# Optimization experiments

Measured on AMD Instinct MI355X. Metric: run time of the kernel, lower is better.

Reference implementation:

```python
import jax, jax.numpy as jnp
import numpy as np
from jax import lax

DROP_PROB = 0.1
BLOCK_SIZE = 7
B, C, H, W = 64, 256, 56, 56
HM, WM = H - (BLOCK_SIZE - 1), W - (BLOCK_SIZE - 1)


def setup_inputs() -> dict:
    key = jax.random.key(0)
    k1, k2 = jax.random.split(key)
    x = jax.random.normal(k1, (B, C, H, W), dtype=jnp.float32)
    mask_u = jax.random.uniform(k2, (B, C, HM, WM), dtype=jnp.float32)
    return {"x": x, "mask_u": mask_u}


def reference(x, mask_u):
    bs = BLOCK_SIZE
    feat = x.shape[2]
    # gamma as in _compute_gamma
    gamma = DROP_PROB / bs**2 * feat**2 / (feat - bs + 1) ** 2
    # Bernoulli(gamma) sample, deterministic given mask_u
    mask = (mask_u < gamma).astype(x.dtype)  # (B,C,HM,WM)
    # The nonzero/scatter block expansion in the original is exactly a
    # stride-1 max-pool with a bs x bs window and (bs-1, bs-1) zero padding,
    # producing the (B,C,H,W) padded dropped-region mask.
    blocked = lax.reduce_window(
        mask, 0.0, lax.max,
        window_dimensions=(1, 1, bs, bs),
        window_strides=(1, 1, 1, 1),
        padding=((0, 0), (0, 0), (bs - 1, bs - 1), (bs - 1, bs - 1)),
    )
    block_mask = 1.0 - blocked  # (B,C,H,W)
    scale = block_mask.size / block_mask.sum()
    return x * block_mask * scale
```

## Files before the change

kernel.cpp:

```cpp
#include <hip/hip_runtime.h>


#define BB 64
#define CC 256
#define HH 56
#define WW 56
#define HMM 50
#define WMM 50
#define BS 7

static constexpr unsigned int NPLANE = BB * CC;
static constexpr unsigned int NTOT   = BB * CC * HH * WW;
static constexpr unsigned int NV     = NTOT / 4;
static constexpr unsigned int PLANEF = HMM * WMM;
static constexpr unsigned int PLANE4 = PLANEF / 4;

typedef float f32x4 __attribute__((ext_vector_type(4)));

__global__ void __launch_bounds__(256) dropblock_mask_kernel(
    const float* __restrict__ mask_u,
    unsigned long long* __restrict__ rowmask,
    unsigned int* __restrict__ plane_cnt,
    float gamma)
{
    const unsigned int tid   = threadIdx.x;
    const unsigned int wid   = tid >> 6;
    const unsigned int lane  = tid & 63u;

    __shared__ float4 lds4[2 * PLANE4];
    const float* lds = reinterpret_cast<const float*>(lds4);

    {
        const float4* src = reinterpret_cast<const float4*>(mask_u)
                          + (size_t)blockIdx.x * (2 * PLANE4);
        #pragma unroll
        for (unsigned int r = 0; r < 5; ++r) {
            unsigned int idx = tid + r * 256u;
            if (idx < 2 * PLANE4) lds4[idx] = src[idx];
        }
    }
    __syncthreads();

    if (wid >= 2) return;

    const unsigned int plane = blockIdx.x * 2u + wid;

    const float* mu = lds + wid * PLANEF;
    unsigned long long my_d = 0ull;

    #pragma unroll
    for (int i = 0; i < HMM; ++i) {
        float v = (lane < WMM) ? mu[i * WMM + lane] : 1.0f;
        unsigned long long m = __ballot(v < gamma);
        unsigned long long d = m | (m << 1);
        d |= d << 2;
        d |= d << 3;
        if (lane == (unsigned)i) my_d = d;
    }

    unsigned long long blocked = my_d;
    blocked |= __shfl_up(blocked, 1, 64);
    blocked |= __shfl_up(blocked, 2, 64);
    blocked |= __shfl_up(blocked, 3, 64);

    if (lane < HH) rowmask[plane * HH + lane] = blocked;

    unsigned int cnt = __popcll(blocked);
    #pragma unroll
    for (int off = 32; off > 0; off >>= 1)
        cnt += __shfl_down(cnt, off, 64);
    if (lane == 0) plane_cnt[plane] = cnt;
}

__global__ void __launch_bounds__(1024) dropblock_scale_kernel(
    const unsigned int* __restrict__ plane_cnt,
    float* __restrict__ scale_out)
{
    __shared__ unsigned int ssum[16];
    const unsigned int t = threadIdx.x;

    const uint4* pc4 = reinterpret_cast<const uint4*>(plane_cnt);
    uint4 a = pc4[t];
    uint4 b = pc4[t + 1024];
    uint4 c = pc4[t + 2048];
    uint4 d = pc4[t + 3072];
    unsigned int s = a.x + a.y + a.z + a.w
                   + b.x + b.y + b.z + b.w
                   + c.x + c.y + c.z + c.w
                   + d.x + d.y + d.z + d.w;

    #pragma unroll
    for (int off = 32; off > 0; off >>= 1)
        s += __shfl_down(s, off, 64);
    if ((t & 63u) == 0u) ssum[t >> 6] = s;
    __syncthreads();

    if (t < 16) {
        unsigned int v = ssum[t];
        #pragma unroll
        for (int off = 8; off > 0; off >>= 1)
            v += __shfl_down(v, off, 64);
        if (t == 0) {
            *scale_out = (float)NTOT / (float)(NTOT - v);
        }
    }
}

__global__ void __launch_bounds__(256) dropblock_apply_kernel(
    const float* __restrict__ x,
    const unsigned long long* __restrict__ rowmask,
    const float* __restrict__ scale_ptr,
    float* __restrict__ out)
{
    unsigned int idx = blockIdx.x * 256u + threadIdx.x;
    if (idx >= NV) return;

    const float scale = *scale_ptr;

    unsigned int plane = idx / (HH * WW / 4);
    unsigned int rem   = idx - plane * (HH * WW / 4);
    unsigned int row   = rem / (WW / 4);
    unsigned int colv  = rem - row * (WW / 4);
    unsigned int col   = colv * 4;

    unsigned long long rm = rowmask[plane * HH + row];
    float4 xv = reinterpret_cast<const float4*>(x)[idx];
    float4 o;
    o.x = ((rm >> (col + 0)) & 1ull) ? 0.0f : xv.x * scale;
    o.y = ((rm >> (col + 1)) & 1ull) ? 0.0f : xv.y * scale;
    o.z = ((rm >> (col + 2)) & 1ull) ? 0.0f : xv.z * scale;
    o.w = ((rm >> (col + 3)) & 1ull) ? 0.0f : xv.w * scale;
    reinterpret_cast<float4*>(out)[idx] = o;
}

extern "C" void kernel_launch(void* const* d_in, const int* in_sizes, int n_in,
                              void* d_out, int out_size, void* d_ws, size_t ws_size,
                              hipStream_t stream) {
    const float* x      = (const float*)d_in[0];
    const float* mask_u = (const float*)d_in[1];
    float* out          = (float*)d_out;

    float* scale_ws             = (float*)d_ws;
    unsigned int* plane_cnt     = (unsigned int*)((char*)d_ws + 64);
    unsigned long long* rowmask = (unsigned long long*)((char*)d_ws + 65600);

    const double gd = 0.1 / ((double)BS * BS) * ((double)HH * HH) /
                      (((double)HH - BS + 1.0) * ((double)HH - BS + 1.0));
    const float gamma = (float)gd;

    dropblock_mask_kernel<<<NPLANE / 2, 256, 0, stream>>>(
        mask_u, rowmask, plane_cnt, gamma);

    dropblock_scale_kernel<<<1, 1024, 0, stream>>>(plane_cnt, scale_ws);

    dropblock_apply_kernel<<<(NV + 255u) / 256u, 256, 0, stream>>>(
        x, rowmask, scale_ws, out);
}
```

Measured before the change: 434.0 us.

## Fuse scale reduction into apply kernel with grid-stride persistent blocks

Removes the single-block scale kernel. The mask kernel now writes one count per block instead of one per plane. Each of 2048 apply blocks redundantly sums the 8192 per-block counts (32 KB) to compute the scale, then walks the tensor with a grid-stride loop. This drops one kernel launch and its serial tail, at the cost of every block repeating a small reduction that should be served from L2.

New measurement: 449.3 us. 3.5% more time.

```diff
diff --git a/kernel.cpp b/kernel.cpp
--- a/kernel.cpp
+++ b/kernel.cpp
@@ -14,20 +14,24 @@
 static constexpr unsigned int NV     = NTOT / 4;
 static constexpr unsigned int PLANEF = HMM * WMM;
 static constexpr unsigned int PLANE4 = PLANEF / 4;
+static constexpr unsigned int MGRID  = NPLANE / 2;
+static constexpr unsigned int AGRID  = 2048;
+static constexpr unsigned int ASTRIDE = AGRID * 256;
 
 typedef float f32x4 __attribute__((ext_vector_type(4)));
 
 __global__ void __launch_bounds__(256) dropblock_mask_kernel(
     const float* __restrict__ mask_u,
     unsigned long long* __restrict__ rowmask,
-    unsigned int* __restrict__ plane_cnt,
+    unsigned int* __restrict__ block_cnt,
     float gamma)
 {
-    const unsigned int tid   = threadIdx.x;
-    const unsigned int wid   = tid >> 6;
-    const unsigned int lane  = tid & 63u;
+    const unsigned int tid  = threadIdx.x;
+    const unsigned int wid  = tid >> 6;
+    const unsigned int lane = tid & 63u;
 
     __shared__ float4 lds4[2 * PLANE4];
+    __shared__ unsigned int csh[2];
     const float* lds = reinterpret_cast<const float*>(lds4);
 
     {
@@ -41,96 +45,89 @@
     }
     __syncthreads();
 
-    if (wid >= 2) return;
+    if (wid < 2) {
+        const unsigned int plane = blockIdx.x * 2u + wid;
 
-    const unsigned int plane = blockIdx.x * 2u + wid;
+        const float* mu = lds + wid * PLANEF;
+        unsigned long long my_d = 0ull;
 
-    const float* mu = lds + wid * PLANEF;
-    unsigned long long my_d = 0ull;
+        #pragma unroll
+        for (int i = 0; i < HMM; ++i) {
+            float v = (lane < WMM) ? mu[i * WMM + lane] : 1.0f;
+            unsigned long long m = __ballot(v < gamma);
+            unsigned long long d = m | (m << 1);
+            d |= d << 2;
+            d |= d << 3;
+            if (lane == (unsigned)i) my_d = d;
+        }
 
-    #pragma unroll
-    for (int i = 0; i < HMM; ++i) {
-        float v = (lane < WMM) ? mu[i * WMM + lane] : 1.0f;
-        unsigned long long m = __ballot(v < gamma);
-        unsigned long long d = m | (m << 1);
-        d |= d << 2;
-        d |= d << 3;
-        if (lane == (unsigned)i) my_d = d;
+        unsigned long long blocked = my_d;
+        blocked |= __shfl_up(blocked, 1, 64);
+        blocked |= __shfl_up(blocked, 2, 64);
+        blocked |= __shfl_up(blocked, 3, 64);
+
+        if (lane < HH) rowmask[plane * HH + lane] = blocked;
+
+        unsigned int cnt = __popcll(blocked);
+        #pragma unroll
+        for (int off = 32; off > 0; off >>= 1)
+            cnt += __shfl_down(cnt, off, 64);
+        if (lane == 0) csh[wid] = cnt;
     }
-
-    unsigned long long blocked = my_d;
-    blocked |= __shfl_up(blocked, 1, 64);
-    blocked |= __shfl_up(blocked, 2, 64);
-    blocked |= __shfl_up(blocked, 3, 64);
-
-    if (lane < HH) rowmask[plane * HH + lane] = blocked;
-
-    unsigned int cnt = __popcll(blocked);
-    #pragma unroll
-    for (int off = 32; off > 0; off >>= 1)
-        cnt += __shfl_down(cnt, off, 64);
-    if (lane == 0) plane_cnt[plane] = cnt;
-}
-
-__global__ void __launch_bounds__(1024) dropblock_scale_kernel(
-    const unsigned int* __restrict__ plane_cnt,
-    float* __restrict__ scale_out)
-{
-    __shared__ unsigned int ssum[16];
-    const unsigned int t = threadIdx.x;
-
-    const uint4* pc4 = reinterpret_cast<const uint4*>(plane_cnt);
-    uint4 a = pc4[t];
-    uint4 b = pc4[t + 1024];
-    uint4 c = pc4[t + 2048];
-    uint4 d = pc4[t + 3072];
-    unsigned int s = a.x + a.y + a.z + a.w
-                   + b.x + b.y + b.z + b.w
-                   + c.x + c.y + c.z + c.w
-                   + d.x + d.y + d.z + d.w;
-
-    #pragma unroll
-    for (int off = 32; off > 0; off >>= 1)
-        s += __shfl_down(s, off, 64);
-    if ((t & 63u) == 0u) ssum[t >> 6] = s;
     __syncthreads();
-
-    if (t < 16) {
-        unsigned int v = ssum[t];
-        #pragma unroll
-        for (int off = 8; off > 0; off >>= 1)
-            v += __shfl_down(v, off, 64);
-        if (t == 0) {
-            *scale_out = (float)NTOT / (float)(NTOT - v);
-        }
-    }
+    if (tid == 0) block_cnt[blockIdx.x] = csh[0] + csh[1];
 }
 
 __global__ void __launch_bounds__(256) dropblock_apply_kernel(
     const float* __restrict__ x,
     const unsigned long long* __restrict__ rowmask,
-    const float* __restrict__ scale_ptr,
+    const unsigned int* __restrict__ block_cnt,
     float* __restrict__ out)
 {
-    unsigned int idx = blockIdx.x * 256u + threadIdx.x;
-    if (idx >= NV) return;
+    const unsigned int tid  = threadIdx.x;
+    const unsigned int wid  = tid >> 6;
+    const unsigned int lane = tid & 63u;
 
-    const float scale = *scale_ptr;
+    __shared__ unsigned int ssum[4];
+    __shared__ float scale_sh;
 
-    unsigned int plane = idx / (HH * WW / 4);
-    unsigned int rem   = idx - plane * (HH * WW / 4);
-    unsigned int row   = rem / (WW / 4);
-    unsigned int colv  = rem - row * (WW / 4);
-    unsigned int col   = colv * 4;
+    {
+        const uint4* c4 = reinterpret_cast<const uint4*>(block_cnt);
+        unsigned int s = 0;
+        #pragma unroll
+        for (unsigned int k = 0; k < 8; ++k) {
+            uint4 v = c4[tid + k * 256u];
+            s += v.x + v.y + v.z + v.w;
+        }
+        #pragma unroll
+        for (int off = 32; off > 0; off >>= 1)
+            s += __shfl_down(s, off, 64);
+        if (lane == 0) ssum[wid] = s;
+        __syncthreads();
+        if (tid == 0) {
+            unsigned int tot = ssum[0] + ssum[1] + ssum[2] + ssum[3];
+            scale_sh = (float)NTOT / (float)(NTOT - tot);
+        }
+        __syncthreads();
+    }
+    const float scale = scale_sh;
 
-    unsigned long long rm = rowmask[plane * HH + row];
-    float4 xv = reinterpret_cast<const float4*>(x)[idx];
-    float4 o;
-    o.x = ((rm >> (col + 0)) & 1ull) ? 0.0f : xv.x * scale;
-    o.y = ((rm >> (col + 1)) & 1ull) ? 0.0f : xv.y * scale;
-    o.z = ((rm >> (col + 2)) & 1ull) ? 0.0f : xv.z * scale;
-    o.w = ((rm >> (col + 3)) & 1ull) ? 0.0f : xv.w * scale;
-    reinterpret_cast<float4*>(out)[idx] = o;
+    for (unsigned int idx = blockIdx.x * 256u + tid; idx < NV; idx += ASTRIDE) {
+        unsigned int plane = idx / (HH * WW / 4);
+        unsigned int rem   = idx - plane * (HH * WW / 4);
+        unsigned int row   = rem / (WW / 4);
+        unsigned int colv  = rem - row * (WW / 4);
+        unsigned int col   = colv * 4;
+
+        unsigned long long rm = rowmask[plane * HH + row];
+        float4 xv = reinterpret_cast<const float4*>(x)[idx];
+        float4 o;
+        o.x = ((rm >> (col + 0)) & 1ull) ? 0.0f : xv.x * scale;
+        o.y = ((rm >> (col + 1)) & 1ull) ? 0.0f : xv.y * scale;
+        o.z = ((rm >> (col + 2)) & 1ull) ? 0.0f : xv.z * scale;
+        o.w = ((rm >> (col + 3)) & 1ull) ? 0.0f : xv.w * scale;
+        reinterpret_cast<float4*>(out)[idx] = o;
+    }
 }
 
 extern "C" void kernel_launch(void* const* d_in, const int* in_sizes, int n_in,
@@ -140,19 +137,16 @@
     const float* mask_u = (const float*)d_in[1];
     float* out          = (float*)d_out;
 
-    float* scale_ws             = (float*)d_ws;
-    unsigned int* plane_cnt     = (unsigned int*)((char*)d_ws + 64);
-    unsigned long long* rowmask = (unsigned long long*)((char*)d_ws + 65600);
+    unsigned int* block_cnt     = (unsigned int*)d_ws;
+    unsigned long long* rowmask = (unsigned long long*)((char*)d_ws + 32768);
 
     const double gd = 0.1 / ((double)BS * BS) * ((double)HH * HH) /
                       (((double)HH - BS + 1.0) * ((double)HH - BS + 1.0));
     const float gamma = (float)gd;
 
-    dropblock_mask_kernel<<<NPLANE / 2, 256, 0, stream>>>(
-        mask_u, rowmask, plane_cnt, gamma);
+    dropblock_mask_kernel<<<MGRID, 256, 0, stream>>>(
+        mask_u, rowmask, block_cnt, gamma);
 
-    dropblock_scale_kernel<<<1, 1024, 0, stream>>>(plane_cnt, scale_ws);
-
-    dropblock_apply_kernel<<<(NV + 255u) / 256u, 256, 0, stream>>>(
-        x, rowmask, scale_ws, out);
+    dropblock_apply_kernel<<<AGRID, 256, 0, stream>>>(
+        x, rowmask, block_cnt, out);
 }
```
